# Performance work log

Hardware: AMD Instinct MI355X
Metric: run time of the kernel (lower is better)

Reference implementation:

```python
import math
import jax, jax.numpy as jnp
import numpy as np

N_HEAD = 8
EPS = 1e-4

def _ln(x, g, b):
    m = jnp.mean(x, axis=-1, keepdims=True)
    v = jnp.mean((x - m) ** 2, axis=-1, keepdims=True)
    return (x - m) * jax.lax.rsqrt(v + EPS) * g + b

def _rel_bias(T, rel_w):
    # rel_pos_mat[i,j] = j - i, shifted to [0, 2T-2]; one-hot @ W == table lookup
    pos = jnp.arange(T)
    idx = pos[None, :] - pos[:, None] + (T - 1)        # [T,T]
    return rel_w[idx].transpose(2, 0, 1)               # [n_head,T,T]

def _attn(x, qw, qb, kw, kb, vw, vb, pw, pb, rel_pos):
    B, T, C = x.shape
    hd = C // N_HEAD
    q = (x @ qw + qb).reshape(B, T, N_HEAD, hd)
    k = (x @ kw + kb).reshape(B, T, N_HEAD, hd)
    v = (x @ vw + vb).reshape(B, T, N_HEAD, hd)
    att = jnp.einsum('bqhd,bkhd->bhqk', q, k) * (1.0 / math.sqrt(hd))
    att = att + rel_pos[None]
    att = jax.nn.softmax(att, axis=-1)
    y = jnp.einsum('bhqk,bkhd->bqhd', att, v).reshape(B, T, C)
    return y @ pw + pb

def setup_inputs() -> dict:
    key = jax.random.key(0)
    C, H, W, B = 512, 64, 64, 8
    ks = iter(jax.random.split(key, 40))
    d = {}
    d['x'] = jax.random.normal(next(ks), (B, H * W, C), jnp.float32)
    def w(shape):
        return jax.random.normal(next(ks), shape, jnp.float32) * 0.02
    for p in ('row', 'col'):
        for nm in ('q', 'k', 'v', 'p'):
            d[f'{p}_{nm}w'] = w((C, C))
            d[f'{p}_{nm}b'] = jnp.zeros((C,), jnp.float32)
    for nm in ('rln1', 'cln1', 'ln2'):
        d[f'{nm}_g'] = jnp.ones((C,), jnp.float32)
        d[f'{nm}_b'] = jnp.zeros((C,), jnp.float32)
    d['ff_w1'] = w((C, 4 * C)); d['ff_b1'] = jnp.zeros((4 * C,), jnp.float32)
    d['ff_w2'] = w((4 * C, C)); d['ff_b2'] = jnp.zeros((C,), jnp.float32)
    d['row_rel_w'] = w((2 * H - 1, N_HEAD))
    d['col_rel_w'] = w((2 * W - 1, N_HEAD))
    return d

def reference(x,
              row_qw, row_qb, row_kw, row_kb, row_vw, row_vb, row_pw, row_pb,
              col_qw, col_qb, col_kw, col_kb, col_vw, col_vb, col_pw, col_pb,
              rln1_g, rln1_b, cln1_g, cln1_b, ln2_g, ln2_b,
              ff_w1, ff_b1, ff_w2, ff_b2, row_rel_w, col_rel_w):
    b, n, c = x.shape
    h = w = int(math.isqrt(n))
    # row attention: over h within each column -> batch b*w
    xr = x.reshape(b, h, w, c).transpose(0, 2, 1, 3).reshape(b * w, h, c)
    x_row = _attn(_ln(xr, rln1_g, rln1_b),
                  row_qw, row_qb, row_kw, row_kb, row_vw, row_vb, row_pw, row_pb,
                  _rel_bias(h, row_rel_w))
    x_row = x_row.reshape(b, w, h, c).transpose(0, 2, 1, 3).reshape(b, h * w, c)
    # col attention: over w within each row -> batch b*h
    xc = xr.reshape(b, w, h, c).transpose(0, 2, 1, 3).reshape(b * h, w, c)
    x_col = _attn(_ln(xc, cln1_g, cln1_b),
                  col_qw, col_qb, col_kw, col_kb, col_vw, col_vb, col_pw, col_pb,
                  _rel_bias(w, col_rel_w))
    x_col = x_col.reshape(b, h * w, c)
    out = x + x_row + x_col
    hdd = _ln(out, ln2_g, ln2_b) @ ff_w1 + ff_b1
    hdd = jax.nn.gelu(hdd, approximate=False)
    out = out + (hdd @ ff_w2 + ff_b2)
    return out
```

## Files before the change

kernel.cpp:

```cpp
#include <hip/hip_runtime.h>

typedef unsigned short u16;
typedef unsigned int   u32;
typedef float  f32x4  __attribute__((ext_vector_type(4)));
typedef u32    u32x4  __attribute__((ext_vector_type(4)));
typedef __bf16 bf16x8 __attribute__((ext_vector_type(8)));

#define DEV __device__ __forceinline__

DEV float b2f(u16 u){ return __uint_as_float(((u32)u) << 16); }
DEV u16 f2b(float f){
  u32 u = __float_as_uint(f);
  u32 r = 0x7FFFu + ((u >> 16) & 1u);
  return (u16)((u + r) >> 16);
}
DEV u32 pack2(float a, float b){ return (u32)f2b(a) | ((u32)f2b(b) << 16); }
DEV uint4 pack8(const float* o){
  uint4 r;
  r.x = pack2(o[0], o[1]); r.y = pack2(o[2], o[3]);
  r.z = pack2(o[4], o[5]); r.w = pack2(o[6], o[7]);
  return r;
}

DEV f32x4 mfma16(u32x4 a, u32x4 b, f32x4 c){
  return __builtin_amdgcn_mfma_f32_16x16x32_bf16(
      __builtin_bit_cast(bf16x8, a), __builtin_bit_cast(bf16x8, b), c, 0, 0, 0);
}

DEV void gload16(const u16* g, u16* l){
  __builtin_amdgcn_global_load_lds((const __attribute__((address_space(1))) void*)(g),
                                   (__attribute__((address_space(3))) void*)(l), 16, 0, 0);
}

__global__ __launch_bounds__(256) void tranb4(
    const float* __restrict__ sA, const float* __restrict__ sB,
    const float* __restrict__ sC, const float* __restrict__ sD,
    u16* __restrict__ dA, u16* __restrict__ dB,
    u16* __restrict__ dC, u16* __restrict__ dD){
  __shared__ float tile[32][33];
  const float* src = (blockIdx.z == 0) ? sA : (blockIdx.z == 1) ? sB
                   : (blockIdx.z == 2) ? sC : sD;
  u16* dst = (blockIdx.z == 0) ? dA : (blockIdx.z == 1) ? dB
           : (blockIdx.z == 2) ? dC : dD;
  const int bx = blockIdx.x * 32, by = blockIdx.y * 32;
  const int tx = threadIdx.x, ty = threadIdx.y;
#pragma unroll
  for (int i = 0; i < 4; ++i)
    tile[ty + i * 8][tx] = src[(size_t)(by + ty + i * 8) * 512 + bx + tx];
  __syncthreads();
#pragma unroll
  for (int i = 0; i < 4; ++i)
    dst[(size_t)(bx + ty + i * 8) * 512 + by + tx] = f2b(tile[tx][ty + i * 8]);
}

__global__ __launch_bounds__(256) void tranb(const float* __restrict__ src, u16* __restrict__ dst,
                                             int R, int C){
  __shared__ float tile[32][33];
  const int bx = blockIdx.x * 32, by = blockIdx.y * 32;
  const int tx = threadIdx.x, ty = threadIdx.y;
#pragma unroll
  for (int i = 0; i < 4; ++i)
    tile[ty + i * 8][tx] = src[(size_t)(by + ty + i * 8) * C + bx + tx];
  __syncthreads();
#pragma unroll
  for (int i = 0; i < 4; ++i)
    dst[(size_t)(bx + ty + i * 8) * R + by + tx] = f2b(tile[tx][ty + i * 8]);
}

__global__ __launch_bounds__(256) void ln_k(const float* __restrict__ x,
    const float* __restrict__ g1, const float* __restrict__ b1,
    u16* __restrict__ y1){
  const int tid = threadIdx.x, lane = tid & 63, wv = tid >> 6;
  const size_t row  = (size_t)blockIdx.x * 4 + wv;
  const size_t boff = row * 512 + lane * 8;
  float f[8];
  {
    const f32x4* p = (const f32x4*)(x + boff);
    const f32x4 a = p[0], b = p[1];
#pragma unroll
    for (int j = 0; j < 4; ++j){ f[j] = a[j]; f[4 + j] = b[j]; }
  }
  float s1 = 0.f, s2 = 0.f;
#pragma unroll
  for (int j = 0; j < 8; ++j){ s1 += f[j]; s2 += f[j] * f[j]; }
#pragma unroll
  for (int off = 32; off > 0; off >>= 1){
    s1 += __shfl_xor(s1, off);
    s2 += __shfl_xor(s2, off);
  }
  const float m   = s1 * (1.0f / 512.0f);
  const float var = s2 * (1.0f / 512.0f) - m * m;
  const float inv = rsqrtf(var + 1e-4f);
  const int cb = lane * 8;
  float o[8];
#pragma unroll
  for (int j = 0; j < 8; ++j) o[j] = (f[j] - m) * inv * g1[cb + j] + b1[cb + j];
  *(uint4*)(y1 + boff) = pack8(o);
}

template<int EPI, bool FUSE3>
__global__ __launch_bounds__(512, 2) void gemm128(const u16* __restrict__ A,
    const u16* __restrict__ Bt,
    const float* __restrict__ b0p, const float* __restrict__ b1p,
    const float* __restrict__ b2p,
    const float* __restrict__ res, void* __restrict__ outv,
    int Nd, int K, int lda){
  __shared__ __align__(16) u16 smem[32768];
  const int tid  = threadIdx.x;
  const int lane = tid & 63;
  const int lr = lane & 15, lg = lane >> 4;
  const int wave = tid >> 6;
  const int wm = (wave >> 2) * 64, wn = (wave & 3) * 32;
  const u32 fd  = blockIdx.y * gridDim.x + blockIdx.x;
  const u32 cpx = (gridDim.x * gridDim.y) >> 3;
  const u32 T   = (fd & 7) * cpx + (fd >> 3);
  const int m0 = (T / gridDim.x) * 128, n0 = (T % gridDim.x) * 128;
  const int nk = K >> 6;

  f32x4 acc[4][2] = {};

  auto stage = [&](int buf, int kt){
    const int kb = kt * 64;
    const int ao = buf * 8192, bo = 16384 + buf * 8192;
#pragma unroll
    for (int i = 0; i < 2; ++i){
      const int c = i * 512 + tid;
      const int r = c >> 3, gc = (c & 7) ^ (r & 7);
      gload16(A + (size_t)(m0 + r) * lda + kb + gc * 8, smem + ao + c * 8);
    }
#pragma unroll
    for (int i = 0; i < 2; ++i){
      const int c = i * 512 + tid;
      const int r = c >> 3, gc = (c & 7) ^ (r & 7);
      gload16(Bt + (size_t)(n0 + r) * K + kb + gc * 8, smem + bo + c * 8);
    }
  };

  stage(0, 0);
  int cur = 0;
  for (int kt = 0; kt < nk; ++kt){
    if (kt + 1 < nk){
      stage(cur ^ 1, kt + 1);
      asm volatile("s_waitcnt vmcnt(4)" ::: "memory");
    } else {
      asm volatile("s_waitcnt vmcnt(0)" ::: "memory");
    }
    __builtin_amdgcn_s_barrier();
    __builtin_amdgcn_sched_barrier(0);
    const int ao = cur * 8192, bo = 16384 + cur * 8192;
#pragma unroll
    for (int kk = 0; kk < 2; ++kk){
      u32x4 af[4], bf[2];
#pragma unroll
      for (int t = 0; t < 4; ++t){
        const int js = (kk * 4 + lg) ^ (lr & 7);
        af[t] = *(const u32x4*)&smem[ao + (wm + t * 16 + lr) * 64 + js * 8];
      }
#pragma unroll
      for (int t = 0; t < 2; ++t){
        const int js = (kk * 4 + lg) ^ (lr & 7);
        bf[t] = *(const u32x4*)&smem[bo + (wn + t * 16 + lr) * 64 + js * 8];
      }
      __builtin_amdgcn_s_setprio(1);
#pragma unroll
      for (int mt = 0; mt < 4; ++mt)
#pragma unroll
        for (int nt = 0; nt < 2; ++nt)
          acc[mt][nt] = mfma16(af[mt], bf[nt], acc[mt][nt]);
      __builtin_amdgcn_s_setprio(0);
    }
    asm volatile("" ::: "memory");
    __builtin_amdgcn_sched_barrier(0);
    __builtin_amdgcn_s_barrier();
    cur ^= 1;
  }

  if (EPI == 2){
    float* Cf = (float*)smem;
#pragma unroll
    for (int mt = 0; mt < 4; ++mt)
#pragma unroll
      for (int nt = 0; nt < 2; ++nt){
        const int col = wn + nt * 16 + lr;
        const float bv = b0p[n0 + col];
#pragma unroll
        for (int r = 0; r < 4; ++r)
          Cf[(wm + mt * 16 + lg * 4 + r) * 128 + col] = acc[mt][nt][r] + bv;
      }
    __syncthreads();
    float* o = (float*)outv;
#pragma unroll
    for (int p = 0; p < 8; ++p){
      const int rr = p * 16 + (tid >> 5);
      const int cc = (tid & 31) * 4;
      f32x4 c = *(f32x4*)&Cf[rr * 128 + cc];
      const size_t gi = (size_t)(m0 + rr) * Nd + n0 + cc;
      c += *(const f32x4*)(res + gi);
      *(f32x4*)(o + gi) = c;
    }
  } else {
    u16* Cl = smem;
#pragma unroll
    for (int mt = 0; mt < 4; ++mt)
#pragma unroll
      for (int nt = 0; nt < 2; ++nt){
        const int col = n0 + wn + nt * 16 + lr;
        float bv;
        if (FUSE3){
          if (col >= 1024)      bv = b2p[col - 1024];
          else if (col >= 512)  bv = b1p[col - 512];
          else                  bv = b0p[col];
        } else bv = b0p[col];
#pragma unroll
        for (int r = 0; r < 4; ++r){
          float v2 = acc[mt][nt][r] + bv;
          if (EPI == 1) v2 = 0.5f * v2 * (1.0f + erff(v2 * 0.70710678118654752f));
          Cl[(wm + mt * 16 + lg * 4 + r) * 136 + wn + nt * 16 + lr] = f2b(v2);
        }
      }
    __syncthreads();
    u16* o = (u16*)outv;
#pragma unroll
    for (int p = 0; p < 4; ++p){
      const int rr = p * 32 + (tid >> 4);
      const int cc = (tid & 15) * 8;
      *(uint4*)(o + (size_t)(m0 + rr) * Nd + n0 + cc) = *(uint4*)&Cl[rr * 136 + cc];
    }
  }
}

__global__ __launch_bounds__(256, 2) void attn64(u16* __restrict__ q,
    const u16* __restrict__ k, const u16* __restrict__ v,
    const float* __restrict__ relw,
    int ldq, int sscale, int tstr){
  __shared__ __align__(16) u16 Qs[64 * 80];
  __shared__ __align__(16) u16 Ks[64 * 80];
  __shared__ __align__(16) u16 Vt[64 * 80];
  __shared__ __align__(16) u16 Ps[64 * 80];
  __shared__ float Ss[64 * 68];
  __shared__ float tb[128];

  const int s = blockIdx.x, head = blockIdx.y;
  const int tid = threadIdx.x;
  const int lane = tid & 63, wv = tid >> 6;
  const int lr = lane & 15, lg = lane >> 4;
  const int base = (s >> 6) * 4096 + (s & 63) * sscale;

  if (tid < 127) tb[tid] = relw[tid * 8 + head];

#pragma unroll
  for (int rep = 0; rep < 2; ++rep){
    const int e = rep * 2048 + tid * 8;
    const int t = e >> 6, c = e & 63;
    const size_t goff = (size_t)(base + t * tstr) * ldq + head * 64 + c;
    *(uint4*)&Qs[t * 80 + c] = *(const uint4*)(q + goff);
    *(uint4*)&Ks[t * 80 + c] = *(const uint4*)(k + goff);
    const uint4 vvv = *(const uint4*)(v + goff);
    u32 w;
    w = vvv.x; Vt[(c + 0) * 80 + t] = (u16)w; Vt[(c + 1) * 80 + t] = (u16)(w >> 16);
    w = vvv.y; Vt[(c + 2) * 80 + t] = (u16)w; Vt[(c + 3) * 80 + t] = (u16)(w >> 16);
    w = vvv.z; Vt[(c + 4) * 80 + t] = (u16)w; Vt[(c + 5) * 80 + t] = (u16)(w >> 16);
    w = vvv.w; Vt[(c + 6) * 80 + t] = (u16)w; Vt[(c + 7) * 80 + t] = (u16)(w >> 16);
  }
  __syncthreads();

  const int i0 = wv * 16;
  u32x4 af[2];
#pragma unroll
  for (int kk = 0; kk < 2; ++kk)
    af[kk] = *(const u32x4*)&Qs[(i0 + lr) * 80 + kk * 32 + lg * 8];
#pragma unroll
  for (int jt = 0; jt < 4; ++jt){
    f32x4 acc = {};
#pragma unroll
    for (int kk = 0; kk < 2; ++kk){
      const u32x4 bf = *(const u32x4*)&Ks[(jt * 16 + lr) * 80 + kk * 32 + lg * 8];
      acc = mfma16(af[kk], bf, acc);
    }
#pragma unroll
    for (int r = 0; r < 4; ++r){
      const int i = i0 + lg * 4 + r;
      const int j = jt * 16 + lr;
      Ss[i * 68 + j] = acc[r] * 0.125f + tb[j - i + 63];
    }
  }
  __syncthreads();

  {
    const int rr = tid >> 2, cp = tid & 3;
    float ev[16];
    float mx = -3.0e38f;
#pragma unroll
    for (int u = 0; u < 16; ++u){ ev[u] = Ss[rr * 68 + cp * 16 + u]; mx = fmaxf(mx, ev[u]); }
    mx = fmaxf(mx, __shfl_xor(mx, 1, 4));
    mx = fmaxf(mx, __shfl_xor(mx, 2, 4));
    float sum = 0.f;
#pragma unroll
    for (int u = 0; u < 16; ++u){ ev[u] = expf(ev[u] - mx); sum += ev[u]; }
    sum += __shfl_xor(sum, 1, 4);
    sum += __shfl_xor(sum, 2, 4);
    const float inv = 1.0f / sum;
#pragma unroll
    for (int u = 0; u < 16; ++u) Ps[rr * 80 + cp * 16 + u] = f2b(ev[u] * inv);
  }
  __syncthreads();

  u32x4 pa[2];
#pragma unroll
  for (int kk = 0; kk < 2; ++kk)
    pa[kk] = *(const u32x4*)&Ps[(i0 + lr) * 80 + kk * 32 + lg * 8];
#pragma unroll
  for (int dt = 0; dt < 4; ++dt){
    f32x4 acc = {};
#pragma unroll
    for (int kk = 0; kk < 2; ++kk){
      const u32x4 bf = *(const u32x4*)&Vt[(dt * 16 + lr) * 80 + kk * 32 + lg * 8];
      acc = mfma16(pa[kk], bf, acc);
    }
#pragma unroll
    for (int r = 0; r < 4; ++r)
      Qs[(i0 + lg * 4 + r) * 80 + dt * 16 + lr] = f2b(acc[r]);
  }
  __syncthreads();

#pragma unroll
  for (int p = 0; p < 2; ++p){
    const int rr = p * 32 + (tid >> 3);
    const int cc = (tid & 7) * 8;
    *(uint4*)(q + (size_t)(base + rr * tstr) * ldq + head * 64 + cc) =
        *(uint4*)&Qs[rr * 80 + cc];
  }
}

extern "C" void kernel_launch(void* const* d_in, const int* in_sizes, int n_in,
                              void* d_out, int out_size, void* d_ws, size_t ws_size,
                              hipStream_t stream){
  const float* x      = (const float*)d_in[0];
  const float* row_qw = (const float*)d_in[1];  const float* row_qb = (const float*)d_in[2];
  const float* row_kw = (const float*)d_in[3];  const float* row_kb = (const float*)d_in[4];
  const float* row_vw = (const float*)d_in[5];  const float* row_vb = (const float*)d_in[6];
  const float* row_pw = (const float*)d_in[7];  const float* row_pb = (const float*)d_in[8];
  const float* col_qw = (const float*)d_in[9];  const float* col_qb = (const float*)d_in[10];
  const float* col_kw = (const float*)d_in[11]; const float* col_kb = (const float*)d_in[12];
  const float* col_vw = (const float*)d_in[13]; const float* col_vb = (const float*)d_in[14];
  const float* col_pw = (const float*)d_in[15]; const float* col_pb = (const float*)d_in[16];
  const float* rg  = (const float*)d_in[17]; const float* rb  = (const float*)d_in[18];
  const float* cg  = (const float*)d_in[19]; const float* cb  = (const float*)d_in[20];
  const float* l2g = (const float*)d_in[21]; const float* l2b = (const float*)d_in[22];
  const float* ffw1 = (const float*)d_in[23]; const float* ffb1 = (const float*)d_in[24];
  const float* ffw2 = (const float*)d_in[25]; const float* ffb2 = (const float*)d_in[26];
  const float* rrel = (const float*)d_in[27]; const float* crel = (const float*)d_in[28];
  float* outp = (float*)d_out;

  const size_t ACT = (size_t)32768 * 512;
  const size_t W55 = (size_t)512 * 512;
  const size_t NEED = (4 * ACT + 8 * W55) * 2;
  if (ws_size < NEED) return;

  u16* B0 = (u16*)d_ws;
  u16* B1 = B0 + ACT;
  u16* s0 = B1 + 3 * ACT;
  u16* s1 = s0 + W55; u16* s2 = s1 + W55; u16* s3 = s2 + W55;
  u16* s4 = s3 + W55;

  const dim3 tpb(32, 8);
  const dim3 gQKV(12, 256);
  const dim3 gProj(4, 256);
  const dim3 gAttn(512, 8);

  tranb4<<<dim3(16, 16, 4), tpb, 0, stream>>>(row_qw, row_kw, row_vw, row_pw,
                                              s0, s1, s2, s3);
  ln_k<<<8192, 256, 0, stream>>>(x, rg, rb, B0);
  gemm128<0, true><<<gQKV, 512, 0, stream>>>(B0, s0, row_qb, row_kb, row_vb,
                                             nullptr, B1, 1536, 512, 512);
  attn64<<<gAttn, 256, 0, stream>>>(B1, B1 + 512, B1 + 1024, rrel, 1536, 1, 64);
  gemm128<2, false><<<gProj, 512, 0, stream>>>(B1, s3, row_pb, nullptr, nullptr,
                                               x, outp, 512, 512, 1536);

  tranb4<<<dim3(16, 16, 4), tpb, 0, stream>>>(col_qw, col_kw, col_vw, col_pw,
                                              s0, s1, s2, s3);
  ln_k<<<8192, 256, 0, stream>>>(x, cg, cb, B0);
  gemm128<0, true><<<gQKV, 512, 0, stream>>>(B0, s0, col_qb, col_kb, col_vb,
                                             nullptr, B1, 1536, 512, 512);
  attn64<<<gAttn, 256, 0, stream>>>(B1, B1 + 512, B1 + 1024, crel, 1536, 64, 1);
  gemm128<2, false><<<gProj, 512, 0, stream>>>(B1, s3, col_pb, nullptr, nullptr,
                                               outp, outp, 512, 512, 1536);

  ln_k<<<8192, 256, 0, stream>>>(outp, l2g, l2b, B0);
  tranb<<<dim3(64, 16), tpb, 0, stream>>>(ffw1, s0, 512, 2048);
  tranb<<<dim3(16, 64), tpb, 0, stream>>>(ffw2, s4, 2048, 512);
  for (int c = 0; c < 2; ++c){
    const size_t ro = (size_t)c * 16384;
    gemm128<1, false><<<dim3(16, 128), 512, 0, stream>>>(B0 + ro * 512, s0, ffb1,
        nullptr, nullptr, nullptr, B1, 2048, 512, 512);
    gemm128<2, false><<<dim3(4, 128), 512, 0, stream>>>(B1, s4, ffb2,
        nullptr, nullptr, outp + ro * 512, outp + ro * 512, 512, 2048, 2048);
  }
}
```

Measured before the change: 507.3 us.

## Fuse row/col layernorms and merge both output projections into one K-concatenated GEMM

Computes both attention-branch layernorms in a single pass over x, and stores Q, K and V in separate contiguous buffers. Both branches' attention outputs are kept, and the two output projections run as one GEMM over a concatenated K dimension with a packed weight, summed biases and the residual. Some intermediates are staged in the output buffer as scratch. This removes an LN read of x and one full fp32 read-modify-write of the output, at the cost of an extra live activation buffer and more complex aliasing.

New measurement: 473.1 us, median of 2. -6.7%, faster.

```diff
diff --git a/kernel.cpp b/kernel.cpp
--- a/kernel.cpp
+++ b/kernel.cpp
@@ -32,16 +32,13 @@
                                    (__attribute__((address_space(3))) void*)(l), 16, 0, 0);
 }
 
-__global__ __launch_bounds__(256) void tranb4(
+__global__ __launch_bounds__(256) void tranb3(
     const float* __restrict__ sA, const float* __restrict__ sB,
-    const float* __restrict__ sC, const float* __restrict__ sD,
-    u16* __restrict__ dA, u16* __restrict__ dB,
-    u16* __restrict__ dC, u16* __restrict__ dD){
+    const float* __restrict__ sC,
+    u16* __restrict__ dA, u16* __restrict__ dB, u16* __restrict__ dC){
   __shared__ float tile[32][33];
-  const float* src = (blockIdx.z == 0) ? sA : (blockIdx.z == 1) ? sB
-                   : (blockIdx.z == 2) ? sC : sD;
-  u16* dst = (blockIdx.z == 0) ? dA : (blockIdx.z == 1) ? dB
-           : (blockIdx.z == 2) ? dC : dD;
+  const float* src = (blockIdx.z == 0) ? sA : (blockIdx.z == 1) ? sB : sC;
+  u16* dst = (blockIdx.z == 0) ? dA : (blockIdx.z == 1) ? dB : dC;
   const int bx = blockIdx.x * 32, by = blockIdx.y * 32;
   const int tx = threadIdx.x, ty = threadIdx.y;
 #pragma unroll
@@ -51,6 +48,20 @@
 #pragma unroll
   for (int i = 0; i < 4; ++i)
     dst[(size_t)(bx + ty + i * 8) * 512 + by + tx] = f2b(tile[tx][ty + i * 8]);
+}
+
+__global__ __launch_bounds__(256) void tranbP(const float* __restrict__ src,
+                                              u16* __restrict__ dst, int off){
+  __shared__ float tile[32][33];
+  const int bx = blockIdx.x * 32, by = blockIdx.y * 32;
+  const int tx = threadIdx.x, ty = threadIdx.y;
+#pragma unroll
+  for (int i = 0; i < 4; ++i)
+    tile[ty + i * 8][tx] = src[(size_t)(by + ty + i * 8) * 512 + bx + tx];
+  __syncthreads();
+#pragma unroll
+  for (int i = 0; i < 4; ++i)
+    dst[(size_t)(bx + ty + i * 8) * 1024 + off + by + tx] = f2b(tile[tx][ty + i * 8]);
 }
 
 __global__ __launch_bounds__(256) void tranb(const float* __restrict__ src, u16* __restrict__ dst,
@@ -67,9 +78,11 @@
     dst[(size_t)(bx + ty + i * 8) * R + by + tx] = f2b(tile[tx][ty + i * 8]);
 }
 
+template<int TWO>
 __global__ __launch_bounds__(256) void ln_k(const float* __restrict__ x,
     const float* __restrict__ g1, const float* __restrict__ b1,
-    u16* __restrict__ y1){
+    const float* __restrict__ g2, const float* __restrict__ b2,
+    u16* __restrict__ y1, u16* __restrict__ y2){
   const int tid = threadIdx.x, lane = tid & 63, wv = tid >> 6;
   const size_t row  = (size_t)blockIdx.x * 4 + wv;
   const size_t boff = row * 512 + lane * 8;
@@ -96,14 +109,21 @@
 #pragma unroll
   for (int j = 0; j < 8; ++j) o[j] = (f[j] - m) * inv * g1[cb + j] + b1[cb + j];
   *(uint4*)(y1 + boff) = pack8(o);
+  if (TWO){
+#pragma unroll
+    for (int j = 0; j < 8; ++j) o[j] = (f[j] - m) * inv * g2[cb + j] + b2[cb + j];
+    *(uint4*)(y2 + boff) = pack8(o);
+  }
 }
 
 template<int EPI, bool FUSE3>
 __global__ __launch_bounds__(512, 2) void gemm128(const u16* __restrict__ A,
+    const u16* __restrict__ A2nd, int nkA,
     const u16* __restrict__ Bt,
     const float* __restrict__ b0p, const float* __restrict__ b1p,
     const float* __restrict__ b2p,
-    const float* __restrict__ res, void* __restrict__ outv,
+    const float* __restrict__ res,
+    void* __restrict__ out0, void* __restrict__ out1, void* __restrict__ out2,
     int Nd, int K, int lda){
   __shared__ __align__(16) u16 smem[32768];
   const int tid  = threadIdx.x;
@@ -120,19 +140,22 @@
   f32x4 acc[4][2] = {};
 
   auto stage = [&](int buf, int kt){
-    const int kb = kt * 64;
+    const u16* Ap; int kb;
+    if (kt < nkA){ Ap = A;    kb = kt * 64; }
+    else         { Ap = A2nd; kb = (kt - nkA) * 64; }
+    const int kbB = kt * 64;
     const int ao = buf * 8192, bo = 16384 + buf * 8192;
 #pragma unroll
     for (int i = 0; i < 2; ++i){
       const int c = i * 512 + tid;
       const int r = c >> 3, gc = (c & 7) ^ (r & 7);
-      gload16(A + (size_t)(m0 + r) * lda + kb + gc * 8, smem + ao + c * 8);
+      gload16(Ap + (size_t)(m0 + r) * lda + kb + gc * 8, smem + ao + c * 8);
     }
 #pragma unroll
     for (int i = 0; i < 2; ++i){
       const int c = i * 512 + tid;
       const int r = c >> 3, gc = (c & 7) ^ (r & 7);
-      gload16(Bt + (size_t)(n0 + r) * K + kb + gc * 8, smem + bo + c * 8);
+      gload16(Bt + (size_t)(n0 + r) * K + kbB + gc * 8, smem + bo + c * 8);
     }
   };
 
@@ -182,13 +205,14 @@
 #pragma unroll
       for (int nt = 0; nt < 2; ++nt){
         const int col = wn + nt * 16 + lr;
-        const float bv = b0p[n0 + col];
+        float bv = b0p[n0 + col];
+        if (b1p) bv += b1p[n0 + col];
 #pragma unroll
         for (int r = 0; r < 4; ++r)
           Cf[(wm + mt * 16 + lg * 4 + r) * 128 + col] = acc[mt][nt][r] + bv;
       }
     __syncthreads();
-    float* o = (float*)outv;
+    float* o = (float*)out0;
 #pragma unroll
     for (int p = 0; p < 8; ++p){
       const int rr = p * 16 + (tid >> 5);
@@ -219,12 +243,19 @@
         }
       }
     __syncthreads();
-    u16* o = (u16*)outv;
+    u16* o = (u16*)out0;
+    int ncol = n0;
+    if (FUSE3){
+      const int grp = n0 >> 9;
+      o = (u16*)(grp == 0 ? out0 : grp == 1 ? out1 : out2);
+      ncol = n0 & 511;
+    }
 #pragma unroll
     for (int p = 0; p < 4; ++p){
       const int rr = p * 32 + (tid >> 4);
       const int cc = (tid & 15) * 8;
-      *(uint4*)(o + (size_t)(m0 + rr) * Nd + n0 + cc) = *(uint4*)&Cl[rr * 136 + cc];
+      *(uint4*)(o + (size_t)(m0 + rr) * (FUSE3 ? 512 : Nd) + ncol + cc) =
+          *(uint4*)&Cl[rr * 136 + cc];
     }
   }
 }
@@ -232,7 +263,7 @@
 __global__ __launch_bounds__(256, 2) void attn64(u16* __restrict__ q,
     const u16* __restrict__ k, const u16* __restrict__ v,
     const float* __restrict__ relw,
-    int ldq, int sscale, int tstr){
+    int sscale, int tstr){
   __shared__ __align__(16) u16 Qs[64 * 80];
   __shared__ __align__(16) u16 Ks[64 * 80];
   __shared__ __align__(16) u16 Vt[64 * 80];
@@ -252,7 +283,7 @@
   for (int rep = 0; rep < 2; ++rep){
     const int e = rep * 2048 + tid * 8;
     const int t = e >> 6, c = e & 63;
-    const size_t goff = (size_t)(base + t * tstr) * ldq + head * 64 + c;
+    const size_t goff = (size_t)(base + t * tstr) * 512 + head * 64 + c;
     *(uint4*)&Qs[t * 80 + c] = *(const uint4*)(q + goff);
     *(uint4*)&Ks[t * 80 + c] = *(const uint4*)(k + goff);
     const uint4 vvv = *(const uint4*)(v + goff);
@@ -327,7 +358,7 @@
   for (int p = 0; p < 2; ++p){
     const int rr = p * 32 + (tid >> 3);
     const int cc = (tid & 7) * 8;
-    *(uint4*)(q + (size_t)(base + rr * tstr) * ldq + head * 64 + cc) =
+    *(uint4*)(q + (size_t)(base + rr * tstr) * 512 + head * 64 + cc) =
         *(uint4*)&Qs[rr * 80 + cc];
   }
 }
@@ -351,49 +382,57 @@
   const float* ffw2 = (const float*)d_in[25]; const float* ffb2 = (const float*)d_in[26];
   const float* rrel = (const float*)d_in[27]; const float* crel = (const float*)d_in[28];
   float* outp = (float*)d_out;
+  u16* outp16 = (u16*)d_out;
 
   const size_t ACT = (size_t)32768 * 512;
   const size_t W55 = (size_t)512 * 512;
   const size_t NEED = (4 * ACT + 8 * W55) * 2;
   if (ws_size < NEED) return;
 
-  u16* B0 = (u16*)d_ws;
-  u16* B1 = B0 + ACT;
-  u16* s0 = B1 + 3 * ACT;
-  u16* s1 = s0 + W55; u16* s2 = s1 + W55; u16* s3 = s2 + W55;
-  u16* s4 = s3 + W55;
+  u16* A0 = (u16*)d_ws;
+  u16* A1 = A0 + ACT;
+  u16* A2 = A1 + ACT;
+  u16* A3 = A2 + ACT;
+  u16* D0 = outp16;
+  u16* D1 = outp16 + ACT;
+  u16* wtb = A3 + ACT;
+  u16* wt_q = wtb;  u16* wt_k = wtb + W55;  u16* wt_v = wtb + 2 * W55;
+  u16* wt_p = wtb + 3 * W55;
+  u16* f1t  = wtb;
+  u16* f2t  = wtb + 4 * W55;
 
   const dim3 tpb(32, 8);
   const dim3 gQKV(12, 256);
   const dim3 gProj(4, 256);
   const dim3 gAttn(512, 8);
 
-  tranb4<<<dim3(16, 16, 4), tpb, 0, stream>>>(row_qw, row_kw, row_vw, row_pw,
-                                              s0, s1, s2, s3);
-  ln_k<<<8192, 256, 0, stream>>>(x, rg, rb, B0);
-  gemm128<0, true><<<gQKV, 512, 0, stream>>>(B0, s0, row_qb, row_kb, row_vb,
-                                             nullptr, B1, 1536, 512, 512);
-  attn64<<<gAttn, 256, 0, stream>>>(B1, B1 + 512, B1 + 1024, rrel, 1536, 1, 64);
-  gemm128<2, false><<<gProj, 512, 0, stream>>>(B1, s3, row_pb, nullptr, nullptr,
-                                               x, outp, 512, 512, 1536);
-
-  tranb4<<<dim3(16, 16, 4), tpb, 0, stream>>>(col_qw, col_kw, col_vw, col_pw,
-                                              s0, s1, s2, s3);
-  ln_k<<<8192, 256, 0, stream>>>(x, cg, cb, B0);
-  gemm128<0, true><<<gQKV, 512, 0, stream>>>(B0, s0, col_qb, col_kb, col_vb,
-                                             nullptr, B1, 1536, 512, 512);
-  attn64<<<gAttn, 256, 0, stream>>>(B1, B1 + 512, B1 + 1024, crel, 1536, 64, 1);
-  gemm128<2, false><<<gProj, 512, 0, stream>>>(B1, s3, col_pb, nullptr, nullptr,
-                                               outp, outp, 512, 512, 1536);
-
-  ln_k<<<8192, 256, 0, stream>>>(outp, l2g, l2b, B0);
-  tranb<<<dim3(64, 16), tpb, 0, stream>>>(ffw1, s0, 512, 2048);
-  tranb<<<dim3(16, 64), tpb, 0, stream>>>(ffw2, s4, 2048, 512);
+  ln_k<1><<<8192, 256, 0, stream>>>(x, rg, rb, cg, cb, A0, D0);
+
+  tranb3<<<dim3(16, 16, 3), tpb, 0, stream>>>(row_qw, row_kw, row_vw, wt_q, wt_k, wt_v);
+  tranbP<<<dim3(16, 16), tpb, 0, stream>>>(row_pw, wt_p, 0);
+  gemm128<0, true><<<gQKV, 512, 0, stream>>>(A0, A0, 99, wt_q, row_qb, row_kb, row_vb,
+                                             nullptr, A1, A2, A3, 512, 512, 512);
+  attn64<<<gAttn, 256, 0, stream>>>(A1, A2, A3, rrel, 1, 64);
+
+  tranb3<<<dim3(16, 16, 3), tpb, 0, stream>>>(col_qw, col_kw, col_vw, wt_q, wt_k, wt_v);
+  tranbP<<<dim3(16, 16), tpb, 0, stream>>>(col_pw, wt_p, 512);
+  gemm128<0, true><<<gQKV, 512, 0, stream>>>(D0, D0, 99, wt_q, col_qb, col_kb, col_vb,
+                                             nullptr, A2, A3, D1, 512, 512, 512);
+  attn64<<<gAttn, 256, 0, stream>>>(A2, A3, D1, crel, 64, 1);
+
+  gemm128<2, false><<<gProj, 512, 0, stream>>>(A1, A2, 8, wt_p, row_pb, col_pb,
+                                               nullptr, x, outp, nullptr, nullptr,
+                                               512, 1024, 512);
+
+  ln_k<0><<<8192, 256, 0, stream>>>(outp, l2g, l2b, nullptr, nullptr, A0, nullptr);
+  tranb<<<dim3(64, 16), tpb, 0, stream>>>(ffw1, f1t, 512, 2048);
+  tranb<<<dim3(16, 64), tpb, 0, stream>>>(ffw2, f2t, 2048, 512);
   for (int c = 0; c < 2; ++c){
     const size_t ro = (size_t)c * 16384;
-    gemm128<1, false><<<dim3(16, 128), 512, 0, stream>>>(B0 + ro * 512, s0, ffb1,
-        nullptr, nullptr, nullptr, B1, 2048, 512, 512);
-    gemm128<2, false><<<dim3(4, 128), 512, 0, stream>>>(B1, s4, ffb2,
-        nullptr, nullptr, outp + ro * 512, outp + ro * 512, 512, 2048, 2048);
-  }
-}
+    gemm128<1, false><<<dim3(16, 128), 512, 0, stream>>>(A0 + ro * 512, A0, 99, f1t,
+        ffb1, nullptr, nullptr, nullptr, A1, nullptr, nullptr, 2048, 512, 512);
+    gemm128<2, false><<<dim3(4, 128), 512, 0, stream>>>(A1, A1, 99, f2t,
+        ffb2, nullptr, nullptr, outp + ro * 512, outp + ro * 512, nullptr, nullptr,
+        512, 2048, 2048);
+  }
+}
```
